# Performance work log

Hardware: AMD Instinct MI355X
Metric: run time of the kernel (lower is better)

## Reference

```python
import jax, jax.numpy as jnp
import numpy as np


def setup_inputs() -> dict:
    key = jax.random.key(0)
    ks = jax.random.split(key, 5)
    B, C, H, W = 4, 256, 64, 64
    Cq = C // 8
    x = jax.random.normal(ks[0], (B, C, H, W), dtype=jnp.float32)
    Wq = jax.random.normal(ks[1], (Cq, C), dtype=jnp.float32) * (1.0 / np.sqrt(C))
    Wk = jax.random.normal(ks[2], (Cq, C), dtype=jnp.float32) * (1.0 / np.sqrt(C))
    Wv = jax.random.normal(ks[3], (C, C), dtype=jnp.float32) * (1.0 / np.sqrt(C))
    bq = jnp.zeros((Cq,), dtype=jnp.float32)
    bk = jnp.zeros((Cq,), dtype=jnp.float32)
    bv = jnp.zeros((C,), dtype=jnp.float32)
    gamma = jnp.ones((1,), dtype=jnp.float32)
    return {"x": x, "Wq": Wq, "bq": bq, "Wk": Wk, "bk": bk, "Wv": Wv, "bv": bv, "gamma": gamma}


def reference(x, Wq, bq, Wk, bk, Wv, bv, gamma):
    B, C, H, W = x.shape
    N = H * W
    xf = x.reshape(B, C, N)                      # (B, C, N)
    # 1x1 convs == per-pixel linear projections over channels
    q = jnp.einsum('dc,bcn->bdn', Wq, xf) + bq[None, :, None]   # (B, C/8, N)
    k = jnp.einsum('dc,bcn->bdn', Wk, xf) + bk[None, :, None]   # (B, C/8, N)
    v = jnp.einsum('dc,bcn->bdn', Wv, xf) + bv[None, :, None]   # (B, C,   N)
    # attention: note original has NO 1/sqrt(d) scaling
    scores = jnp.einsum('bdn,bdm->bnm', q, k)     # (B, N, N)
    attn = jax.nn.softmax(scores, axis=-1)
    out = jnp.einsum('bnm,bdm->bnd', attn, v)     # (B, N, C)
    out = out.transpose(0, 2, 1).reshape(B, C, H, W)
    return gamma * out + x
```

## Files before the change

kernel.cpp:

```cpp
#include <hip/hip_runtime.h>

#define BATCH 4
#define CH    256
#define DQ    32
#define NPIX  4096
#define LOG2E 1.44269504088896340736f

typedef unsigned short u16;
typedef unsigned int   u32;
typedef __attribute__((ext_vector_type(8))) short short8;
typedef __attribute__((ext_vector_type(16))) float f32x16;

__device__ __align__(16) u16 g_wbf[10 * 2 * 8192];
__device__ float g_bias[10 * 32];

__device__ __forceinline__ float b2f(u32 u) {
  union { u32 i; float f; } v; v.i = (u & 0xffffu) << 16; return v.f;
}
__device__ __forceinline__ u16 f2b(float f) {
  union { float f; u32 i; } v; v.f = f;
  u32 x = v.i; x += 0x7fffu + ((x >> 16) & 1u);
  return (u16)(x >> 16);
}
__device__ __forceinline__ float fexp2(float x) {
#if __has_builtin(__builtin_amdgcn_exp2f)
  return __builtin_amdgcn_exp2f(x);
#else
  return __expf(x * 0.69314718055994530942f);
#endif
}

__device__ __forceinline__ void half_swap(u32 a0, u32 a1, u32 b0, u32 b1,
                                          int hl, uint4& o) {
#if __has_builtin(__builtin_amdgcn_permlane32_swap)
  const auto r0 = __builtin_amdgcn_permlane32_swap((int)a0, (int)b0, false, false);
  const auto r1 = __builtin_amdgcn_permlane32_swap((int)a1, (int)b1, false, false);
  o.x = (u32)r0[0]; o.y = (u32)r1[0]; o.z = (u32)r0[1]; o.w = (u32)r1[1];
#else
  const u32 s0 = hl ? a0 : b0;
  const u32 s1 = hl ? a1 : b1;
  const u32 r0 = (u32)__shfl_xor((int)s0, 32);
  const u32 r1 = (u32)__shfl_xor((int)s1, 32);
  o.x = hl ? r0 : a0; o.y = hl ? r1 : a1;
  o.z = hl ? b0 : r0; o.w = hl ? b1 : r1;
#endif
}

__global__ __launch_bounds__(256) void wprep(
    const float* __restrict__ Wq, const float* __restrict__ bq,
    const float* __restrict__ Wk, const float* __restrict__ bk,
    const float* __restrict__ Wv, const float* __restrict__ bv)
{
  const int jt = blockIdx.x, t = threadIdx.x;
  const float* Wsrc; const float* bsrc; int jrow0; float scale = 1.f;
  if (jt == 0)      { Wsrc = Wq; bsrc = bq; jrow0 = 0; scale = LOG2E; }
  else if (jt == 1) { Wsrc = Wk; bsrc = bk; jrow0 = 0; }
  else              { Wsrc = Wv; bsrc = bv; jrow0 = (jt - 2) * 32; }

  u16* wdst = g_wbf + (size_t)jt * 16384;
  for (int i = 0; i < 32; ++i) {
    const int flat = i * 256 + t;
    const int j = flat >> 8, e = flat & 255;
    const float v = Wsrc[(size_t)(jrow0 + j) * CH + e] * scale;
    const u16 hi = f2b(v);
    const u16 lo = f2b(v - b2f(hi));
    const int idx = (((e >> 4) * 2 + ((e >> 3) & 1)) * 32 + j) * 8 + (e & 7);
    wdst[idx] = hi; wdst[8192 + idx] = lo;
  }
  if (t < 32) g_bias[jt * 32 + t] = bsrc[jrow0 + t] * scale;
}

__global__ __launch_bounds__(256) void xprep(
    const float* __restrict__ x, u16* __restrict__ xt_hi, u16* __restrict__ xt_lo)
{
  const int nt = blockIdx.x, kb4 = blockIdx.y * 4, b = blockIdx.z;
  const int n0 = nt * 128, c0 = blockIdx.y * 64;
  const int t = threadIdx.x;
  __shared__ u32 xls[64][129];

  const int tn = t & 127, cp = t >> 7;
  for (int i = 0; i < 32; ++i) {
    const int c = cp + 2 * i;
    const float v = x[((size_t)b * CH + c0 + c) * NPIX + n0 + tn];
    const u16 h = f2b(v);
    const u16 l = f2b(v - b2f(h));
    xls[c][tn] = (u32)h | ((u32)l << 16);
  }
  __syncthreads();

  for (int rep = 0; rep < 4; ++rep) {
    const int id = t + 256 * rep;
    const int kkhl = id >> 7, n = id & 127;
    union { short8 s; uint4 u; } vh, vl;
    #pragma unroll
    for (int j = 0; j < 8; ++j) {
      const u32 p = xls[kkhl * 8 + j][n];
      vh.s[j] = (short)(p & 0xffffu);
      vl.s[j] = (short)(p >> 16);
    }
    const size_t o = ((((size_t)(b * 32 + nt) * 16 + kb4 + (kkhl >> 1)) * 2
                       + (kkhl & 1)) * 128 + n) * 8;
    *(uint4*)(xt_hi + o) = vh.u;
    *(uint4*)(xt_lo + o) = vl.u;
  }
}

__global__ __launch_bounds__(256, 4) void proj(
    const u16* __restrict__ xt_hi, const u16* __restrict__ xt_lo,
    u16* __restrict__ q_t, u16* __restrict__ k_t, u16* __restrict__ v_swz)
{
  const int nt = blockIdx.x, jt = blockIdx.y, b = blockIdx.z;
  const int t = threadIdx.x;
  const int w = t >> 6, lane = t & 63, hl = lane >> 5, l31 = lane & 31;
  const int nb = w * 32 + l31, n = nt * 128 + nb;

  const u16* __restrict__ wb = g_wbf + (size_t)jt * 16384;
  const size_t xtile = (size_t)(b * 32 + nt) * 16 * 2 * 128 * 8;
  const u16* __restrict__ xh = xt_hi + xtile;
  const u16* __restrict__ xl = xt_lo + xtile;

  f32x16 acc1, acc2;
  #pragma unroll
  for (int r = 0; r < 16; ++r) { acc1[r] = 0.f; acc2[r] = 0.f; }

  #pragma unroll
  for (int kk = 0; kk < 16; ++kk) {
    const int aoff = ((kk * 2 + hl) * 32 + l31) * 8;
    const short8 wah = *(const short8*)(wb + aoff);
    const short8 wal = *(const short8*)(wb + 8192 + aoff);
    const int boff = ((kk * 2 + hl) * 128 + nb) * 8;
    const short8 xbh = *(const short8*)(xh + boff);
    const short8 xbl = *(const short8*)(xl + boff);
    acc1 = __builtin_amdgcn_mfma_f32_32x32x16_bf16(wah, xbh, acc1, 0, 0, 0);
    acc2 = __builtin_amdgcn_mfma_f32_32x32x16_bf16(wah, xbl, acc2, 0, 0, 0);
    acc2 = __builtin_amdgcn_mfma_f32_32x32x16_bf16(wal, xbh, acc2, 0, 0, 0);
  }

  f32x16 accv;
  #pragma unroll
  for (int r = 0; r < 16; ++r)
    accv[r] = acc1[r] + acc2[r]
            + g_bias[jt * 32 + (r & 3) + 8 * (r >> 2) + 4 * hl];

  if (jt <= 1) {
    u16* dst = (jt == 0) ? q_t : k_t;
    #pragma unroll
    for (int r2 = 0; r2 < 4; ++r2) {
      uint2 pk;
      pk.x = (u32)f2b(accv[4 * r2 + 0]) | ((u32)f2b(accv[4 * r2 + 1]) << 16);
      pk.y = (u32)f2b(accv[4 * r2 + 2]) | ((u32)f2b(accv[4 * r2 + 3]) << 16);
      *(uint2*)(dst + ((size_t)b * NPIX + n) * DQ + 4 * hl + 8 * r2) = pk;
    }
  } else {
    const int mc = nt * 4 + w;
    const int kc = (l31 >> 4) & 1, h3 = (l31 >> 3) & 1, j8 = l31 & 7;
    u16* dst = v_swz + (((((size_t)b * 128 + mc) * 8 + (jt - 2)) * 2 + kc) * 2 + h3) * 256 + j8;
    #pragma unroll
    for (int r = 0; r < 16; ++r) {
      const int c5 = (r & 3) + 8 * (r >> 2) + 4 * hl;
      dst[c5 * 8] = f2b(accv[r]);
    }
  }
}

__global__ __launch_bounds__(256, 2) void attn(
    const u16* __restrict__ q_t, const u16* __restrict__ k_t,
    const u16* __restrict__ v_swz, const float* __restrict__ x,
    const float* __restrict__ gamma, float* __restrict__ out)
{
  const int b = blockIdx.y, t = threadIdx.x;
  const int w = t >> 6, lane = t & 63, hl = lane >> 5, l31 = lane & 31;
  const int n0 = blockIdx.x * 32;

  __shared__ float cbuf[8192];
  __shared__ float lbuf[4][64];

  short8 qf[2];
  #pragma unroll
  for (int kd = 0; kd < 2; ++kd)
    qf[kd] = *(const short8*)(q_t + ((size_t)b * NPIX + n0 + l31) * DQ + kd * 16 + hl * 8);

  f32x16 acc[8];
  #pragma unroll
  for (int ct = 0; ct < 8; ++ct)
    #pragma unroll
    for (int r = 0; r < 16; ++r) acc[ct][r] = 0.f;
  float lrun = 0.f;

  const u16* __restrict__ kb = k_t + (size_t)b * NPIX * DQ;

  short8 kf0 = *(const short8*)(kb + ((w * 32) * 32 + l31) * DQ + hl * 8);
  short8 kf1 = *(const short8*)(kb + ((w * 32) * 32 + l31) * DQ + 16 + hl * 8);
  f32x16 st;
  #pragma unroll
  for (int r = 0; r < 16; ++r) st[r] = 0.f;
  st = __builtin_amdgcn_mfma_f32_32x32x16_bf16(kf0, qf[0], st, 0, 0, 0);
  st = __builtin_amdgcn_mfma_f32_32x32x16_bf16(kf1, qf[1], st, 0, 0, 0);
  kf0 = *(const short8*)(kb + ((w * 32 + 1) * 32 + l31) * DQ + hl * 8);
  kf1 = *(const short8*)(kb + ((w * 32 + 1) * 32 + l31) * DQ + 16 + hl * 8);

  #pragma unroll 1
  for (int cc = 0; cc < 32; ++cc) {
    const int mc = w * 32 + cc;
    const size_t vbase = ((size_t)b * 128 + mc) * 8192;

    u32 pk[4][2];
    #pragma unroll
    for (int g = 0; g < 4; ++g) {
      const float e0 = fexp2(st[4 * g + 0]);
      const float e1 = fexp2(st[4 * g + 1]);
      const float e2 = fexp2(st[4 * g + 2]);
      const float e3 = fexp2(st[4 * g + 3]);
      lrun += (e0 + e1) + (e2 + e3);
      pk[g][0] = (u32)f2b(e0) | ((u32)f2b(e1) << 16);
      pk[g][1] = (u32)f2b(e2) | ((u32)f2b(e3) << 16);
    }

    #pragma unroll
    for (int r = 0; r < 16; ++r) st[r] = 0.f;
    st = __builtin_amdgcn_mfma_f32_32x32x16_bf16(kf0, qf[0], st, 0, 0, 0);
    st = __builtin_amdgcn_mfma_f32_32x32x16_bf16(kf1, qf[1], st, 0, 0, 0);

    {
      const int mcp = w * 32 + ((cc < 30) ? cc + 2 : 31);
      kf0 = *(const short8*)(kb + (mcp * 32 + l31) * DQ + hl * 8);
      kf1 = *(const short8*)(kb + (mcp * 32 + l31) * DQ + 16 + hl * 8);
    }

    #pragma unroll
    for (int kc = 0; kc < 2; ++kc) {
      union { uint4 u; short8 s; } bu;
      half_swap(pk[2 * kc][0], pk[2 * kc][1], pk[2 * kc + 1][0], pk[2 * kc + 1][1], hl, bu.u);
      __builtin_amdgcn_s_setprio(1);
      #pragma unroll
      for (int ct = 0; ct < 8; ++ct) {
        const short8 av = *(const short8*)(v_swz + vbase + (size_t)(((ct * 2 + kc) * 2 + hl) * 256) + l31 * 8);
        acc[ct] = __builtin_amdgcn_mfma_f32_32x32x16_bf16(av, bu.s, acc[ct], 0, 0, 0);
      }
      __builtin_amdgcn_s_setprio(0);
    }
  }

  lbuf[w][lane] = lrun;
  __syncthreads();
  for (int src = 1; src < 4; ++src) {
    if (w == src) {
      #pragma unroll
      for (int ct = 0; ct < 8; ++ct)
        #pragma unroll
        for (int r = 0; r < 16; ++r)
          cbuf[(ct * 16 + r) * 64 + lane] = acc[ct][r];
    }
    __syncthreads();
    if (w == 0) {
      #pragma unroll
      for (int ct = 0; ct < 8; ++ct)
        #pragma unroll
        for (int r = 0; r < 16; ++r)
          acc[ct][r] += cbuf[(ct * 16 + r) * 64 + lane];
    }
    __syncthreads();
  }

  if (w == 0) {
    float l = (lbuf[0][lane] + lbuf[1][lane]) + (lbuf[2][lane] + lbuf[3][lane]);
    l += __shfl_xor(l, 32);
    const float linv = 1.0f / l;
    const float g = gamma[0];
    #pragma unroll
    for (int ct = 0; ct < 8; ++ct)
      #pragma unroll
      for (int r = 0; r < 16; ++r) {
        const int c = ct * 32 + (r & 3) + 8 * (r >> 2) + 4 * hl;
        const size_t idx = ((size_t)b * CH + c) * NPIX + n0 + l31;
        out[idx] = g * acc[ct][r] * linv + x[idx];
      }
  }
}

extern "C" void kernel_launch(void* const* d_in, const int* in_sizes, int n_in,
                              void* d_out, int out_size, void* d_ws, size_t ws_size,
                              hipStream_t stream) {
  const float* x  = (const float*)d_in[0];
  const float* Wq = (const float*)d_in[1];
  const float* bq = (const float*)d_in[2];
  const float* Wk = (const float*)d_in[3];
  const float* bk = (const float*)d_in[4];
  const float* Wv = (const float*)d_in[5];
  const float* bv = (const float*)d_in[6];
  const float* gm = (const float*)d_in[7];
  float* out = (float*)d_out;

  const size_t qk_elems = (size_t)BATCH * NPIX * DQ;
  const size_t v_elems  = (size_t)BATCH * NPIX * CH;
  const size_t need = (2 * qk_elems + v_elems) * sizeof(u16);
  if (ws_size < need) return;

  u16* q_t   = (u16*)d_ws;
  u16* k_t   = q_t + qk_elems;
  u16* v_swz = k_t + qk_elems;

  u16* xt_hi = (u16*)d_out;
  u16* xt_lo = xt_hi + (size_t)BATCH * NPIX * CH;

  wprep<<<dim3(10), 256, 0, stream>>>(Wq, bq, Wk, bk, Wv, bv);
  xprep<<<dim3(NPIX / 128, CH / 64, BATCH), 256, 0, stream>>>(x, xt_hi, xt_lo);
  proj<<<dim3(32, 10, BATCH), 256, 0, stream>>>(xt_hi, xt_lo, q_t, k_t, v_swz);
  attn<<<dim3(NPIX / 32, BATCH), 256, 0, stream>>>(q_t, k_t, v_swz, x, gm, out);
}
```

Baseline: 186.9 us.

## Merge weight prep into xprep, remap blocks per XCD, simplify attn K pipeline

Folds the weight-conversion kernel into xprep as an extra z-slice, which removes one kernel launch. Proj and attn now use a flattened 1D grid whose block index is decoded so that blocks sharing a batch (and, in proj, a weight tile) land on the same XCD, aiming for better L2 reuse. In attn, the software-pipelined K load and score MFMA, together with the s_setprio hints, are replaced by a plain in-loop load and compute. That may expose K-load latency in exchange for lower register pressure.

```diff
diff --git a/kernel.cpp b/kernel.cpp
--- a/kernel.cpp
+++ b/kernel.cpp
@@ -46,36 +46,37 @@
 #endif
 }
 
-__global__ __launch_bounds__(256) void wprep(
+__global__ __launch_bounds__(256) void xprep(
+    const float* __restrict__ x, u16* __restrict__ xt_hi, u16* __restrict__ xt_lo,
     const float* __restrict__ Wq, const float* __restrict__ bq,
     const float* __restrict__ Wk, const float* __restrict__ bk,
     const float* __restrict__ Wv, const float* __restrict__ bv)
 {
-  const int jt = blockIdx.x, t = threadIdx.x;
-  const float* Wsrc; const float* bsrc; int jrow0; float scale = 1.f;
-  if (jt == 0)      { Wsrc = Wq; bsrc = bq; jrow0 = 0; scale = LOG2E; }
-  else if (jt == 1) { Wsrc = Wk; bsrc = bk; jrow0 = 0; }
-  else              { Wsrc = Wv; bsrc = bv; jrow0 = (jt - 2) * 32; }
-
-  u16* wdst = g_wbf + (size_t)jt * 16384;
-  for (int i = 0; i < 32; ++i) {
-    const int flat = i * 256 + t;
-    const int j = flat >> 8, e = flat & 255;
-    const float v = Wsrc[(size_t)(jrow0 + j) * CH + e] * scale;
-    const u16 hi = f2b(v);
-    const u16 lo = f2b(v - b2f(hi));
-    const int idx = (((e >> 4) * 2 + ((e >> 3) & 1)) * 32 + j) * 8 + (e & 7);
-    wdst[idx] = hi; wdst[8192 + idx] = lo;
-  }
-  if (t < 32) g_bias[jt * 32 + t] = bsrc[jrow0 + t] * scale;
-}
-
-__global__ __launch_bounds__(256) void xprep(
-    const float* __restrict__ x, u16* __restrict__ xt_hi, u16* __restrict__ xt_lo)
-{
+  const int t = threadIdx.x;
+
+  if (blockIdx.z == BATCH) {
+    if (blockIdx.y != 0 || blockIdx.x >= 10) return;
+    const int jt = blockIdx.x;
+    const float* Wsrc; const float* bsrc; int jrow0; float scale = 1.f;
+    if (jt == 0)      { Wsrc = Wq; bsrc = bq; jrow0 = 0; scale = LOG2E; }
+    else if (jt == 1) { Wsrc = Wk; bsrc = bk; jrow0 = 0; }
+    else              { Wsrc = Wv; bsrc = bv; jrow0 = (jt - 2) * 32; }
+    u16* wdst = g_wbf + (size_t)jt * 16384;
+    for (int i = 0; i < 32; ++i) {
+      const int flat = i * 256 + t;
+      const int j = flat >> 8, e = flat & 255;
+      const float v = Wsrc[(size_t)(jrow0 + j) * CH + e] * scale;
+      const u16 hi = f2b(v);
+      const u16 lo = f2b(v - b2f(hi));
+      const int idx = (((e >> 4) * 2 + ((e >> 3) & 1)) * 32 + j) * 8 + (e & 7);
+      wdst[idx] = hi; wdst[8192 + idx] = lo;
+    }
+    if (t < 32) g_bias[jt * 32 + t] = bsrc[jrow0 + t] * scale;
+    return;
+  }
+
   const int nt = blockIdx.x, kb4 = blockIdx.y * 4, b = blockIdx.z;
   const int n0 = nt * 128, c0 = blockIdx.y * 64;
-  const int t = threadIdx.x;
   __shared__ u32 xls[64][129];
 
   const int tn = t & 127, cp = t >> 7;
@@ -109,7 +110,12 @@
     const u16* __restrict__ xt_hi, const u16* __restrict__ xt_lo,
     u16* __restrict__ q_t, u16* __restrict__ k_t, u16* __restrict__ v_swz)
 {
-  const int nt = blockIdx.x, jt = blockIdx.y, b = blockIdx.z;
+  const int L = blockIdx.x;
+  const int xcd = L & 7, s = L >> 3;
+  const int jt = s >> 4;
+  const int pair = xcd * 16 + (s & 15);
+  const int nt = pair >> 2, b = pair & 3;
+
   const int t = threadIdx.x;
   const int w = t >> 6, lane = t & 63, hl = lane >> 5, l31 = lane & 31;
   const int nb = w * 32 + l31, n = nt * 128 + nb;
@@ -168,9 +174,14 @@
     const u16* __restrict__ v_swz, const float* __restrict__ x,
     const float* __restrict__ gamma, float* __restrict__ out)
 {
-  const int b = blockIdx.y, t = threadIdx.x;
+  const int L = blockIdx.x;
+  const int xcd = L & 7, slot = L >> 3;
+  const int b = xcd >> 1;
+  const int nt = slot * 2 + (xcd & 1);
+  const int n0 = nt * 32;
+
+  const int t = threadIdx.x;
   const int w = t >> 6, lane = t & 63, hl = lane >> 5, l31 = lane & 31;
-  const int n0 = blockIdx.x * 32;
 
   __shared__ float cbuf[8192];
   __shared__ float lbuf[4][64];
@@ -187,22 +198,16 @@
     for (int r = 0; r < 16; ++r) acc[ct][r] = 0.f;
   float lrun = 0.f;
 
-  const u16* __restrict__ kb = k_t + (size_t)b * NPIX * DQ;
-
-  short8 kf0 = *(const short8*)(kb + ((w * 32) * 32 + l31) * DQ + hl * 8);
-  short8 kf1 = *(const short8*)(kb + ((w * 32) * 32 + l31) * DQ + 16 + hl * 8);
-  f32x16 st;
-  #pragma unroll
-  for (int r = 0; r < 16; ++r) st[r] = 0.f;
-  st = __builtin_amdgcn_mfma_f32_32x32x16_bf16(kf0, qf[0], st, 0, 0, 0);
-  st = __builtin_amdgcn_mfma_f32_32x32x16_bf16(kf1, qf[1], st, 0, 0, 0);
-  kf0 = *(const short8*)(kb + ((w * 32 + 1) * 32 + l31) * DQ + hl * 8);
-  kf1 = *(const short8*)(kb + ((w * 32 + 1) * 32 + l31) * DQ + 16 + hl * 8);
-
-  #pragma unroll 1
   for (int cc = 0; cc < 32; ++cc) {
     const int mc = w * 32 + cc;
-    const size_t vbase = ((size_t)b * 128 + mc) * 8192;
+
+    const short8 kf0 = *(const short8*)(k_t + ((size_t)b * NPIX + mc * 32 + l31) * DQ + hl * 8);
+    const short8 kf1 = *(const short8*)(k_t + ((size_t)b * NPIX + mc * 32 + l31) * DQ + 16 + hl * 8);
+    f32x16 st;
+    #pragma unroll
+    for (int r = 0; r < 16; ++r) st[r] = 0.f;
+    st = __builtin_amdgcn_mfma_f32_32x32x16_bf16(kf0, qf[0], st, 0, 0, 0);
+    st = __builtin_amdgcn_mfma_f32_32x32x16_bf16(kf1, qf[1], st, 0, 0, 0);
 
     u32 pk[4][2];
     #pragma unroll
@@ -216,28 +221,16 @@
       pk[g][1] = (u32)f2b(e2) | ((u32)f2b(e3) << 16);
     }
 
-    #pragma unroll
-    for (int r = 0; r < 16; ++r) st[r] = 0.f;
-    st = __builtin_amdgcn_mfma_f32_32x32x16_bf16(kf0, qf[0], st, 0, 0, 0);
-    st = __builtin_amdgcn_mfma_f32_32x32x16_bf16(kf1, qf[1], st, 0, 0, 0);
-
-    {
-      const int mcp = w * 32 + ((cc < 30) ? cc + 2 : 31);
-      kf0 = *(const short8*)(kb + (mcp * 32 + l31) * DQ + hl * 8);
-      kf1 = *(const short8*)(kb + (mcp * 32 + l31) * DQ + 16 + hl * 8);
-    }
-
+    const size_t vbase = ((size_t)b * 128 + mc) * 8192;
     #pragma unroll
     for (int kc = 0; kc < 2; ++kc) {
       union { uint4 u; short8 s; } bu;
       half_swap(pk[2 * kc][0], pk[2 * kc][1], pk[2 * kc + 1][0], pk[2 * kc + 1][1], hl, bu.u);
-      __builtin_amdgcn_s_setprio(1);
       #pragma unroll
       for (int ct = 0; ct < 8; ++ct) {
         const short8 av = *(const short8*)(v_swz + vbase + (size_t)(((ct * 2 + kc) * 2 + hl) * 256) + l31 * 8);
         acc[ct] = __builtin_amdgcn_mfma_f32_32x32x16_bf16(av, bu.s, acc[ct], 0, 0, 0);
       }
-      __builtin_amdgcn_s_setprio(0);
     }
   }
 
@@ -303,8 +296,8 @@
   u16* xt_hi = (u16*)d_out;
   u16* xt_lo = xt_hi + (size_t)BATCH * NPIX * CH;
 
-  wprep<<<dim3(10), 256, 0, stream>>>(Wq, bq, Wk, bk, Wv, bv);
-  xprep<<<dim3(NPIX / 128, CH / 64, BATCH), 256, 0, stream>>>(x, xt_hi, xt_lo);
-  proj<<<dim3(32, 10, BATCH), 256, 0, stream>>>(xt_hi, xt_lo, q_t, k_t, v_swz);
-  attn<<<dim3(NPIX / 32, BATCH), 256, 0, stream>>>(q_t, k_t, v_swz, x, gm, out);
-}
+  xprep<<<dim3(NPIX / 128, CH / 64, BATCH + 1), 256, 0, stream>>>(
+      x, xt_hi, xt_lo, Wq, bq, Wk, bk, Wv, bv);
+  proj<<<dim3(32 * 10 * BATCH), 256, 0, stream>>>(xt_hi, xt_lo, q_t, k_t, v_swz);
+  attn<<<dim3((NPIX / 32) * BATCH), 256, 0, stream>>>(q_t, k_t, v_swz, x, gm, out);
+}
```

Result: faster. 160.3 us (-14.2%).
